# Kernel tuning notes

Measured on AMD Instinct MI355X. Metric: run time of the kernel, lower is better.

Reference implementation:

```python
import jax, jax.numpy as jnp
import numpy as np

GROUP_SIZE = 128

def _dequantize(qweight, wscales, wzeros):
    # qweight: [N, K//2] packed bytes, two uint4 values per byte
    # low nibble = even k index, high nibble = odd k index
    N, Kh = qweight.shape
    K = Kh * 2
    low = qweight & 0xF
    high = (qweight >> 4) & 0xF
    w_int = jnp.stack([low, high], axis=-1).reshape(N, K).astype(jnp.float32)  # [N, K]
    G = K // GROUP_SIZE  # number of groups along K
    w_grp = w_int.reshape(N, G, GROUP_SIZE)
    s = wscales.T.reshape(N, G, 1)   # wscales: [G, N] -> [N, G, 1]
    z = wzeros.T.reshape(N, G, 1)
    return ((w_grp - z) * s).reshape(N, K)  # [N, K] dequantized

def setup_inputs() -> dict:
    key = jax.random.key(0)
    k1, k2, k3, k4, k5 = jax.random.split(key, 5)
    M, K, N = 4096, 4096, 12288
    G = K // GROUP_SIZE
    x = jax.random.normal(k1, (M, K), dtype=jnp.float32)
    qweight = jax.random.randint(k2, (N, K // 2), 0, 256, dtype=jnp.int32)
    wscales = jax.random.uniform(k3, (G, N), dtype=jnp.float32) * 0.05
    wzeros = jax.random.uniform(k4, (G, N), dtype=jnp.float32) * 15.0
    bias = jax.random.normal(k5, (N,), dtype=jnp.float32)
    return {"x": x, "qweight": qweight, "wscales": wscales, "wzeros": wzeros, "bias": bias}

def reference(x, qweight, wscales, wzeros, bias):
    # AWQ W4A16 linear: y = x @ dequant(W)^T + b
    w = _dequantize(qweight, wscales, wzeros)  # [N, K]
    return jnp.einsum('mk,nk->mn', x, w) + bias
```

## Files before the change

kernel.cpp:

```cpp
#include <hip/hip_runtime.h>

#define M_DIM 4096
#define K_DIM 4096
#define N_DIM 12288
#define BM 128
#define BN 128
#define BK 64

typedef __bf16 bf16x8 __attribute__((ext_vector_type(8)));
typedef float  floatx4 __attribute__((ext_vector_type(4)));

__global__ __launch_bounds__(256) void xcast_kernel(const float* __restrict__ x,
                                                    __bf16* __restrict__ xb) {
    int idx = blockIdx.x * 256 + threadIdx.x;
    const float4* xv = (const float4*)x;
    float4 a = xv[idx * 2];
    float4 b = xv[idx * 2 + 1];
    bf16x8 o;
    o[0] = (__bf16)a.x; o[1] = (__bf16)a.y; o[2] = (__bf16)a.z; o[3] = (__bf16)a.w;
    o[4] = (__bf16)b.x; o[5] = (__bf16)b.y; o[6] = (__bf16)b.z; o[7] = (__bf16)b.w;
    ((bf16x8*)xb)[idx] = o;
}

__global__ __launch_bounds__(256) void dequant_kernel(const int* __restrict__ qw,
                                                      const float* __restrict__ scales,
                                                      const float* __restrict__ zeros,
                                                      __bf16* __restrict__ wb) {
    int idx = blockIdx.x * 256 + threadIdx.x;
    int n  = idx >> 9;
    int jq = (idx & 511) << 2;
    int g  = jq >> 6;
    float s = scales[g * N_DIM + n];
    float z = zeros[g * N_DIM + n];
    int4 q = *(const int4*)(qw + (size_t)n * (K_DIM / 2) + jq);
    bf16x8 o;
    o[0] = (__bf16)(((float)(q.x & 15)        - z) * s);
    o[1] = (__bf16)(((float)((q.x >> 4) & 15) - z) * s);
    o[2] = (__bf16)(((float)(q.y & 15)        - z) * s);
    o[3] = (__bf16)(((float)((q.y >> 4) & 15) - z) * s);
    o[4] = (__bf16)(((float)(q.z & 15)        - z) * s);
    o[5] = (__bf16)(((float)((q.z >> 4) & 15) - z) * s);
    o[6] = (__bf16)(((float)(q.w & 15)        - z) * s);
    o[7] = (__bf16)(((float)((q.w >> 4) & 15) - z) * s);
    *(bf16x8*)(wb + (size_t)n * K_DIM + (size_t)jq * 2) = o;
}

__global__ __launch_bounds__(256, 2) void gemm_kernel(const __bf16* __restrict__ A,
                                                      const __bf16* __restrict__ B,
                                                      const float* __restrict__ bias,
                                                      float* __restrict__ C) {
    __shared__ __bf16 As[BM * BK];
    __shared__ __bf16 Bs[BN * BK];

    const int tid  = threadIdx.x;
    const int wave = tid >> 6;
    const int lane = tid & 63;
    const int quad = lane >> 4;
    const int l16  = lane & 15;
    const int wm = (wave >> 1) * 64;
    const int wn = (wave & 1) * 64;
    const int bm0 = blockIdx.y * BM;
    const int bn0 = blockIdx.x * BN;

    const int rowInChunk = lane >> 3;
    const int kblk       = (lane & 7) ^ rowInChunk;
    const int kOffElem   = kblk * 8;

    floatx4 acc[4][4] = {};

    for (int kt = 0; kt < K_DIM / BK; ++kt) {
        const int k0 = kt * BK;
        #pragma unroll
        for (int r = 0; r < 4; ++r) {
            const int chunk = wave * 4 + r;
            const int row   = chunk * 8 + rowInChunk;
            const __bf16* ga = A + (size_t)(bm0 + row) * K_DIM + k0 + kOffElem;
            const __bf16* gb = B + (size_t)(bn0 + row) * K_DIM + k0 + kOffElem;
            __builtin_amdgcn_global_load_lds(
                (const __attribute__((address_space(1))) void*)ga,
                (__attribute__((address_space(3))) void*)(As + chunk * 8 * BK), 16, 0, 0);
            __builtin_amdgcn_global_load_lds(
                (const __attribute__((address_space(1))) void*)gb,
                (__attribute__((address_space(3))) void*)(Bs + chunk * 8 * BK), 16, 0, 0);
        }
        __syncthreads();

        #pragma unroll
        for (int ks = 0; ks < 2; ++ks) {
            bf16x8 af[4], bfr[4];
            const int kx = (ks << 2) | quad;
            #pragma unroll
            for (int i = 0; i < 4; ++i) {
                const int ar = wm + i * 16 + l16;
                const int br = wn + i * 16 + l16;
                af[i]  = *(const bf16x8*)(As + ar * BK + ((kx ^ (l16 & 7)) << 3));
                bfr[i] = *(const bf16x8*)(Bs + br * BK + ((kx ^ (l16 & 7)) << 3));
            }
            #pragma unroll
            for (int mi = 0; mi < 4; ++mi)
                #pragma unroll
                for (int ni = 0; ni < 4; ++ni)
                    acc[mi][ni] = __builtin_amdgcn_mfma_f32_16x16x32_bf16(
                        af[mi], bfr[ni], acc[mi][ni], 0, 0, 0);
        }
        __syncthreads();
    }

    #pragma unroll
    for (int ni = 0; ni < 4; ++ni) {
        const int col = bn0 + wn + ni * 16 + l16;
        const float bv = bias[col];
        #pragma unroll
        for (int mi = 0; mi < 4; ++mi) {
            #pragma unroll
            for (int r = 0; r < 4; ++r) {
                const int row = bm0 + wm + mi * 16 + quad * 4 + r;
                C[(size_t)row * N_DIM + col] = acc[mi][ni][r] + bv;
            }
        }
    }
}

extern "C" void kernel_launch(void* const* d_in, const int* in_sizes, int n_in,
                              void* d_out, int out_size, void* d_ws, size_t ws_size,
                              hipStream_t stream) {
    const float* x      = (const float*)d_in[0];
    const int*   qw     = (const int*)d_in[1];
    const float* scales = (const float*)d_in[2];
    const float* zeros  = (const float*)d_in[3];
    const float* bias   = (const float*)d_in[4];
    float* out = (float*)d_out;

    __bf16* xb = (__bf16*)d_ws;
    __bf16* wb = (__bf16*)((char*)d_ws + (size_t)M_DIM * K_DIM * 2);

    xcast_kernel<<<(M_DIM * K_DIM / 8) / 256, 256, 0, stream>>>(x, xb);
    dequant_kernel<<<(N_DIM * (K_DIM / 2) / 4) / 256, 256, 0, stream>>>(qw, scales, zeros, wb);

    dim3 grid(N_DIM / BN, M_DIM / BM);
    gemm_kernel<<<grid, 256, 0, stream>>>(xb, wb, bias, out);
}
```

Measured before the change: 744.7 us.

## Switch GEMM to 32x32x16 MFMA and swap grid order to M-major

Replaces the 4x4 grid of 16x16x32 bf16 MFMAs per wave with a 2x2 grid of 32x32x16 MFMAs. This halves the LDS fragment loads per k-step and uses the larger matrix instruction, with accumulator and epilogue index mapping rewritten to match. It also swaps the block grid so blockIdx.x walks M tiles, which changes which tiles run concurrently and how L2 reuse of A versus B plays out. The risk is that the new lane and register-to-row mapping or the LDS swizzle becomes bank-conflicted or mis-indexed.

```diff
diff --git a/kernel.cpp b/kernel.cpp
--- a/kernel.cpp
+++ b/kernel.cpp
@@ -7,8 +7,8 @@
 #define BN 128
 #define BK 64
 
-typedef __bf16 bf16x8 __attribute__((ext_vector_type(8)));
-typedef float  floatx4 __attribute__((ext_vector_type(4)));
+typedef __bf16 bf16x8  __attribute__((ext_vector_type(8)));
+typedef float  floatx16 __attribute__((ext_vector_type(16)));
 
 __global__ __launch_bounds__(256) void xcast_kernel(const float* __restrict__ x,
                                                     __bf16* __restrict__ xb) {
@@ -55,18 +55,18 @@
     const int tid  = threadIdx.x;
     const int wave = tid >> 6;
     const int lane = tid & 63;
-    const int quad = lane >> 4;
-    const int l16  = lane & 15;
+    const int l32  = lane & 31;
+    const int half = lane >> 5;
     const int wm = (wave >> 1) * 64;
     const int wn = (wave & 1) * 64;
-    const int bm0 = blockIdx.y * BM;
-    const int bn0 = blockIdx.x * BN;
+    const int bm0 = blockIdx.x * BM;
+    const int bn0 = blockIdx.y * BN;
 
     const int rowInChunk = lane >> 3;
     const int kblk       = (lane & 7) ^ rowInChunk;
     const int kOffElem   = kblk * 8;
 
-    floatx4 acc[4][4] = {};
+    floatx16 acc[2][2] = {};
 
     for (int kt = 0; kt < K_DIM / BK; ++kt) {
         const int k0 = kt * BK;
@@ -86,36 +86,36 @@
         __syncthreads();
 
         #pragma unroll
-        for (int ks = 0; ks < 2; ++ks) {
-            bf16x8 af[4], bfr[4];
-            const int kx = (ks << 2) | quad;
+        for (int ks = 0; ks < 4; ++ks) {
+            bf16x8 af[2], bfr[2];
+            const int blk = ks * 2 + half;
             #pragma unroll
-            for (int i = 0; i < 4; ++i) {
-                const int ar = wm + i * 16 + l16;
-                const int br = wn + i * 16 + l16;
-                af[i]  = *(const bf16x8*)(As + ar * BK + ((kx ^ (l16 & 7)) << 3));
-                bfr[i] = *(const bf16x8*)(Bs + br * BK + ((kx ^ (l16 & 7)) << 3));
+            for (int t = 0; t < 2; ++t) {
+                const int ra = wm + t * 32 + l32;
+                const int rb = wn + t * 32 + l32;
+                af[t]  = *(const bf16x8*)(As + ra * BK + ((blk ^ (ra & 7)) << 3));
+                bfr[t] = *(const bf16x8*)(Bs + rb * BK + ((blk ^ (rb & 7)) << 3));
             }
             #pragma unroll
-            for (int mi = 0; mi < 4; ++mi)
+            for (int mi = 0; mi < 2; ++mi)
                 #pragma unroll
-                for (int ni = 0; ni < 4; ++ni)
-                    acc[mi][ni] = __builtin_amdgcn_mfma_f32_16x16x32_bf16(
+                for (int ni = 0; ni < 2; ++ni)
+                    acc[mi][ni] = __builtin_amdgcn_mfma_f32_32x32x16_bf16(
                         af[mi], bfr[ni], acc[mi][ni], 0, 0, 0);
         }
         __syncthreads();
     }
 
     #pragma unroll
-    for (int ni = 0; ni < 4; ++ni) {
-        const int col = bn0 + wn + ni * 16 + l16;
+    for (int ni = 0; ni < 2; ++ni) {
+        const int col = bn0 + wn + ni * 32 + l32;
         const float bv = bias[col];
         #pragma unroll
-        for (int mi = 0; mi < 4; ++mi) {
+        for (int mi = 0; mi < 2; ++mi) {
             #pragma unroll
-            for (int r = 0; r < 4; ++r) {
-                const int row = bm0 + wm + mi * 16 + quad * 4 + r;
-                C[(size_t)row * N_DIM + col] = acc[mi][ni][r] + bv;
+            for (int reg = 0; reg < 16; ++reg) {
+                const int row = bm0 + wm + mi * 32 + half * 4 + (reg & 3) + 8 * (reg >> 2);
+                C[(size_t)row * N_DIM + col] = acc[mi][ni][reg] + bv;
             }
         }
     }
@@ -137,6 +137,6 @@
     xcast_kernel<<<(M_DIM * K_DIM / 8) / 256, 256, 0, stream>>>(x, xb);
     dequant_kernel<<<(N_DIM * (K_DIM / 2) / 4) / 256, 256, 0, stream>>>(qw, scales, zeros, wb);
 
-    dim3 grid(N_DIM / BN, M_DIM / BM);
+    dim3 grid(M_DIM / BM, N_DIM / BN);
     gemm_kernel<<<grid, 256, 0, stream>>>(xb, wb, bias, out);
 }
```

After: 696.4 us. 6.5% less time.
